# Kernel optimization log

Hardware: AMD Instinct MI355X
Metric: run time of the kernel (lower is better)

The kernel has to match this reference:

```python
import jax, jax.numpy as jnp
import numpy as np

N_NODES = 100000
N_EDGES = 1600000
IN_F, HID, N_COLORS = 128, 128, 10


def setup_inputs() -> dict:
    key = jax.random.key(0)
    k1, k2, k3, k4 = jax.random.split(key, 4)
    x = jax.random.normal(k1, (N_NODES, IN_F), dtype=jnp.float32)
    edge_index = jax.random.randint(k2, (2, N_EDGES), 0, N_NODES, dtype=jnp.int64)
    # Glorot-ish init for weights
    W1 = jax.random.normal(k3, (IN_F, HID), dtype=jnp.float32) / np.sqrt(IN_F)
    b1 = jnp.zeros((HID,), dtype=jnp.float32)
    W2 = jax.random.normal(k4, (HID, N_COLORS), dtype=jnp.float32) / np.sqrt(HID)
    b2 = jnp.zeros((N_COLORS,), dtype=jnp.float32)
    return {"x": x, "edge_index": edge_index, "W1": W1, "b1": b1, "W2": W2, "b2": b2}


def _gcn_norm(edge_index, num_nodes):
    # Add self-loops, compute symmetric normalization D^-1/2 (A+I) D^-1/2
    loops = jnp.arange(num_nodes, dtype=edge_index.dtype)
    src = jnp.concatenate([edge_index[0], loops])
    dst = jnp.concatenate([edge_index[1], loops])
    deg = jax.ops.segment_sum(jnp.ones_like(dst, dtype=jnp.float32), dst,
                              num_segments=num_nodes)
    deg_isqrt = jax.lax.rsqrt(deg)  # deg >= 1 due to self-loops
    norm = deg_isqrt[src] * deg_isqrt[dst]  # [E + N]
    return src, dst, norm


def _gcn_conv(h, src, dst, norm, num_nodes, W, b):
    # Linear transform first (PyG GCNConv), then gather-scale-scatter aggregate
    h = h @ W                                   # [N, out]
    msg = h[src] * norm[:, None]                # [E + N, out] gather
    out = jax.ops.segment_sum(msg, dst, num_segments=num_nodes)  # scatter-add
    return out + b


def reference(x, edge_index, W1, b1, W2, b2):
    n = x.shape[0]
    src, dst, norm = _gcn_norm(edge_index, n)
    h = _gcn_conv(x, src, dst, norm, n, W1, b1)
    h = jax.nn.relu(h)
    # dropout is identity in eval mode
    h = _gcn_conv(h, src, dst, norm, n, W2, b2)
    return jax.nn.softmax(h, axis=1)
```

## Files before the change

### kernel.cpp

```cpp
#include <hip/hip_runtime.h>
#include <hip/hip_fp16.h>

#define IN_F 128
#define HID  128
#define NC   10
#define H2P  16
#define NPB  128
#define NBMAX 784
#define BCAP 2560
#define CAPP 2944
#define EPB  4096
#define LDW  136

typedef _Float16 f16x8 __attribute__((ext_vector_type(8)));
typedef float f32x4 __attribute__((ext_vector_type(4)));
typedef int int4a __attribute__((ext_vector_type(4), aligned(4)));

__device__ inline __half2 shfl_xor_h2(__half2 v, int mask) {
    int i = __shfl_xor(*reinterpret_cast<int*>(&v), mask, 64);
    return *reinterpret_cast<__half2*>(&i);
}

__global__ __launch_bounds__(1024) void k_bin(const int* __restrict__ src,
                                              const int* __restrict__ dst,
                                              int* __restrict__ bcnt,
                                              unsigned int* __restrict__ binned,
                                              const float* __restrict__ W1,
                                              __half* __restrict__ WT,
                                              const float* __restrict__ W2,
                                              float* __restrict__ W2T,
                                              int E, int nbin) {
    __shared__ int hist[NBMAX];
    __shared__ int base[NBMAX];
    __shared__ int lcur[NBMAX];
    const int tid = threadIdx.x;

    if (blockIdx.x == 0) {
        for (int i = tid; i < IN_F * HID; i += 1024) {
            int k = i >> 7, n = i & 127;
            WT[n * IN_F + k] = __float2half(W1[k * HID + n]);
        }
        for (int i = tid; i < NC * IN_F; i += 1024)
            W2T[i] = W2[(i & 127) * NC + (i >> 7)];
    }

    for (int b = tid; b < nbin; b += 1024) { hist[b] = 0; lcur[b] = 0; }
    __syncthreads();

    const int e0 = blockIdx.x * EPB + tid;
    int d[4];
    #pragma unroll
    for (int u = 0; u < 4; u++) {
        int e = e0 + u * 1024;
        d[u] = (e < E) ? dst[e] : -1;
        if (d[u] >= 0) atomicAdd(&hist[d[u] >> 7], 1);
    }
    __syncthreads();
    for (int b = tid; b < nbin; b += 1024) {
        int h = hist[b];
        base[b] = h ? atomicAdd(&bcnt[b], h) : 0;
    }
    __syncthreads();
    #pragma unroll
    for (int u = 0; u < 4; u++) {
        int e = e0 + u * 1024;
        if (e < E) {
            int dd = d[u];
            int b = dd >> 7;
            int s = src[e];
            int o = base[b] + atomicAdd(&lcur[b], 1);
            if (o < BCAP)
                binned[(size_t)b * BCAP + o] = ((unsigned)(dd & 127) << 17) | (unsigned)s;
        }
    }
}

__global__ __launch_bounds__(256) void k_pg(const int* __restrict__ bcnt,
                                            const unsigned int* __restrict__ binned,
                                            int2* __restrict__ rowinfo,
                                            float* __restrict__ dis,
                                            int* __restrict__ csr,
                                            const float* __restrict__ X,
                                            const __half* __restrict__ WT,
                                            __half* __restrict__ hsh,
                                            __half* __restrict__ h2h,
                                            int N) {
    __shared__ int h[NPB];
    __shared__ int lb[NPB];
    __shared__ int cur[NPB];
    __shared__ float sdis[NPB];
    __shared__ _Float16 sX[32 * LDW];
    __shared__ _Float16 sW[128 * LDW];
    const int b = blockIdx.x;
    const int tid = threadIdx.x;

    if (tid < NPB) h[tid] = 0;
    __syncthreads();

    const int m = min(bcnt[b], BCAP);
    const unsigned int* p = binned + (size_t)b * BCAP;
    for (int i = tid; i < m; i += 256) atomicAdd(&h[p[i] >> 17], 1);
    __syncthreads();

    int myh = 0, cnt4 = 0;
    if (tid < NPB) { myh = h[tid]; cnt4 = (myh + 3) & ~3; lb[tid] = cnt4; }
    __syncthreads();
    #pragma unroll
    for (int off = 1; off < NPB; off <<= 1) {
        int t = (tid < NPB && tid >= off) ? lb[tid - off] : 0;
        __syncthreads();
        if (tid < NPB) lb[tid] += t;
        __syncthreads();
    }
    int ex = 0;
    if (tid < NPB) {
        ex = lb[tid] - cnt4;
        int node = b * NPB + tid;
        if (node < N) {
            rowinfo[node] = make_int2(b * CAPP + ex, cnt4);
            float dd = rsqrtf(1.0f + (float)myh);
            dis[node] = dd;
            sdis[tid] = dd;
        }
        lb[tid] = ex;
        cur[tid] = 0;
    }
    __syncthreads();
    for (int i = tid; i < m; i += 256) {
        unsigned v = p[i];
        int dl = v >> 17;
        int r = atomicAdd(&cur[dl], 1);
        csr[b * CAPP + lb[dl] + r] = (int)(v & 0x1FFFF);
    }
    if (tid < NPB) {
        for (int k = myh; k < cnt4; k++) csr[b * CAPP + ex + k] = N;
    }
    if (b == 0) {
        f16x8 z = {0, 0, 0, 0, 0, 0, 0, 0};
        if (tid < 16) *(f16x8*)(hsh + (size_t)N * HID + tid * 8) = z;
        if (tid < 2)  *(f16x8*)(h2h + (size_t)N * H2P + tid * 8) = z;
    }

    {
        int n = tid >> 1, part = tid & 1;
        const f16x8* srcp = (const f16x8*)(WT + n * IN_F + part * 64);
        f16x8* dstp = (f16x8*)(sW + n * LDW + part * 64);
        #pragma unroll
        for (int c = 0; c < 8; c++) dstp[c] = srcp[c];
    }
    const int wave = tid >> 6;
    const int lane = tid & 63;
    const int quad = lane >> 4;
    const int l16 = lane & 15;
    const int nbase = wave * 32;

    for (int tdx = 0; tdx < 4; tdx++) {
        int row0 = b * NPB + tdx * 32;
        if (row0 >= N) break;
        __syncthreads();
        {
            int r = tid >> 3;
            int k0 = (tid & 7) * 16;
            const float* sp = X + (size_t)(row0 + r) * IN_F + k0;
            float4 f0 = *(const float4*)(sp);
            float4 f1 = *(const float4*)(sp + 4);
            float4 f2 = *(const float4*)(sp + 8);
            float4 f3 = *(const float4*)(sp + 12);
            f16x8 h0, h1;
            h0[0] = (_Float16)f0.x; h0[1] = (_Float16)f0.y;
            h0[2] = (_Float16)f0.z; h0[3] = (_Float16)f0.w;
            h0[4] = (_Float16)f1.x; h0[5] = (_Float16)f1.y;
            h0[6] = (_Float16)f1.z; h0[7] = (_Float16)f1.w;
            h1[0] = (_Float16)f2.x; h1[1] = (_Float16)f2.y;
            h1[2] = (_Float16)f2.z; h1[3] = (_Float16)f2.w;
            h1[4] = (_Float16)f3.x; h1[5] = (_Float16)f3.y;
            h1[6] = (_Float16)f3.z; h1[7] = (_Float16)f3.w;
            *(f16x8*)(sX + r * LDW + k0) = h0;
            *(f16x8*)(sX + r * LDW + k0 + 8) = h1;
        }
        __syncthreads();

        f32x4 acc00 = {0,0,0,0}, acc01 = {0,0,0,0}, acc10 = {0,0,0,0}, acc11 = {0,0,0,0};
        #pragma unroll
        for (int kc = 0; kc < 4; kc++) {
            const int koff = kc * 32 + quad * 8;
            f16x8 a0 = *(const f16x8*)(sX + l16 * LDW + koff);
            f16x8 a1 = *(const f16x8*)(sX + (16 + l16) * LDW + koff);
            f16x8 b0 = *(const f16x8*)(sW + (nbase + l16) * LDW + koff);
            f16x8 b1 = *(const f16x8*)(sW + (nbase + 16 + l16) * LDW + koff);
            acc00 = __builtin_amdgcn_mfma_f32_16x16x32_f16(a0, b0, acc00, 0, 0, 0);
            acc01 = __builtin_amdgcn_mfma_f32_16x16x32_f16(a0, b1, acc01, 0, 0, 0);
            acc10 = __builtin_amdgcn_mfma_f32_16x16x32_f16(a1, b0, acc10, 0, 0, 0);
            acc11 = __builtin_amdgcn_mfma_f32_16x16x32_f16(a1, b1, acc11, 0, 0, 0);
        }
        #pragma unroll
        for (int r = 0; r < 4; r++) {
            {
                int lr = tdx * 32 + quad * 4 + r;
                float d = sdis[lr];
                __half* o = hsh + (size_t)(b * NPB + lr) * HID + nbase + l16;
                o[0]  = __float2half(acc00[r] * d);
                o[16] = __float2half(acc01[r] * d);
            }
            {
                int lr = tdx * 32 + 16 + quad * 4 + r;
                float d = sdis[lr];
                __half* o = hsh + (size_t)(b * NPB + lr) * HID + nbase + l16;
                o[0]  = __float2half(acc10[r] * d);
                o[16] = __float2half(acc11[r] * d);
            }
        }
    }
}

__global__ __launch_bounds__(256) void k_agg1(const __half* __restrict__ hsh,
                                              const int2* __restrict__ rowinfo,
                                              const int* __restrict__ csr,
                                              const float* __restrict__ dis,
                                              const float* __restrict__ b1,
                                              const float* __restrict__ W2T,
                                              __half* __restrict__ h2h,
                                              int N) {
    const int node = blockIdx.x * 4 + (threadIdx.x >> 6);
    if (node >= N) return;
    const int lane = threadIdx.x & 63;
    const int g   = lane >> 4;
    const int l16 = lane & 15;
    const int f0  = l16 * 8;
    const __half2 hz = __half2half2(__float2half(0.0f));

    const int2 ri = rowinfo[node];
    const int beg = ri.x, end = ri.x + ri.y;
    const float d = dis[node];

    __half2 acc2[4] = {hz, hz, hz, hz};
    if (g == 0) {
        float4 r = *(const float4*)(hsh + (size_t)node * HID + f0);
        const __half2* hh = (const __half2*)&r;
        acc2[0] = hh[0]; acc2[1] = hh[1]; acc2[2] = hh[2]; acc2[3] = hh[3];
    }

    int j0 = beg + 4 * g;
    if (j0 < end) {
        int4a cv0 = *(const int4a*)(csr + j0);
        int  j1 = j0 + 16;
        bool m1 = j1 < end;
        int4a cv1 = m1 ? *(const int4a*)(csr + j1) : cv0;
        float4 r0 = *(const float4*)(hsh + (size_t)cv0[0] * HID + f0);
        float4 r1 = *(const float4*)(hsh + (size_t)cv0[1] * HID + f0);
        float4 r2 = *(const float4*)(hsh + (size_t)cv0[2] * HID + f0);
        float4 r3 = *(const float4*)(hsh + (size_t)cv0[3] * HID + f0);
        while (true) {
            const int  j2 = j1 + 16;
            const bool m2 = m1 && (j2 < end);
            int4a cv2 = m2 ? *(const int4a*)(csr + j2) : cv1;
            float4 n0, n1, n2, n3;
            if (m1) {
                n0 = *(const float4*)(hsh + (size_t)cv1[0] * HID + f0);
                n1 = *(const float4*)(hsh + (size_t)cv1[1] * HID + f0);
                n2 = *(const float4*)(hsh + (size_t)cv1[2] * HID + f0);
                n3 = *(const float4*)(hsh + (size_t)cv1[3] * HID + f0);
            }
            const __half2* h0 = (const __half2*)&r0;
            const __half2* h1 = (const __half2*)&r1;
            const __half2* h2 = (const __half2*)&r2;
            const __half2* h3 = (const __half2*)&r3;
            #pragma unroll
            for (int i = 0; i < 4; i++) {
                acc2[i] = __hadd2(acc2[i], h0[i]);
                acc2[i] = __hadd2(acc2[i], h1[i]);
                acc2[i] = __hadd2(acc2[i], h2[i]);
                acc2[i] = __hadd2(acc2[i], h3[i]);
            }
            if (!m1) break;
            r0 = n0; r1 = n1; r2 = n2; r3 = n3;
            cv1 = cv2; m1 = m2; j1 = j2;
        }
    }

    #pragma unroll
    for (int i = 0; i < 4; i++) {
        acc2[i] = __hadd2(acc2[i], shfl_xor_h2(acc2[i], 16));
        acc2[i] = __hadd2(acc2[i], shfl_xor_h2(acc2[i], 32));
    }
    float acc[8];
    #pragma unroll
    for (int i = 0; i < 4; i++) {
        float2 t = __half22float2(acc2[i]);
        acc[2 * i] = t.x; acc[2 * i + 1] = t.y;
    }

    float4 ba = *(const float4*)(b1 + f0);
    float4 bb = *(const float4*)(b1 + f0 + 4);
    float h[8];
    h[0] = fmaxf(fmaf(d, acc[0], ba.x), 0.0f);
    h[1] = fmaxf(fmaf(d, acc[1], ba.y), 0.0f);
    h[2] = fmaxf(fmaf(d, acc[2], ba.z), 0.0f);
    h[3] = fmaxf(fmaf(d, acc[3], ba.w), 0.0f);
    h[4] = fmaxf(fmaf(d, acc[4], bb.x), 0.0f);
    h[5] = fmaxf(fmaf(d, acc[5], bb.y), 0.0f);
    h[6] = fmaxf(fmaf(d, acc[6], bb.z), 0.0f);
    h[7] = fmaxf(fmaf(d, acc[7], bb.w), 0.0f);

    const int cb = (g == 0) ? 0 : (g == 1) ? 3 : (g == 2) ? 6 : 8;
    const int nc = (g < 2) ? 3 : 2;
    float p[3];
    #pragma unroll
    for (int ci = 0; ci < 3; ci++) {
        if (ci < nc) {
            int c = cb + ci;
            float4 wa = *(const float4*)(W2T + c * IN_F + f0);
            float4 wb = *(const float4*)(W2T + c * IN_F + f0 + 4);
            float t = fmaf(h[0], wa.x, fmaf(h[1], wa.y, fmaf(h[2], wa.z, h[3] * wa.w)));
            t = fmaf(h[4], wb.x, fmaf(h[5], wb.y, fmaf(h[6], wb.z, fmaf(h[7], wb.w, t))));
            #pragma unroll
            for (int off = 1; off < 16; off <<= 1) t += __shfl_xor(t, off, 64);
            p[ci] = t;
        }
    }
    if (l16 == 0) {
        __half* o = h2h + (size_t)node * H2P + cb;
        for (int ci = 0; ci < nc; ci++) o[ci] = __float2half(d * p[ci]);
    }
}

__global__ __launch_bounds__(256) void k_agg2(const __half* __restrict__ h2h,
                                              const int2* __restrict__ rowinfo,
                                              const int* __restrict__ csr,
                                              const float* __restrict__ dis,
                                              const float* __restrict__ b2,
                                              float* __restrict__ out,
                                              int N) {
    int t = blockIdx.x * 256 + threadIdx.x;
    int node = t >> 3;
    if (node >= N) return;
    int o = t & 7;
    int q = o & 1;
    int eg = o >> 1;
    const int base = q * 8;
    const __half2 hz = __half2half2(__float2half(0.0f));

    __half2 a2[4] = {hz, hz, hz, hz};
    if (eg == 0) {
        float4 r = *(const float4*)(h2h + (size_t)node * H2P + base);
        const __half2* hh = (const __half2*)&r;
        a2[0] = hh[0]; a2[1] = hh[1]; a2[2] = hh[2]; a2[3] = hh[3];
    }
    const int2 ri = rowinfo[node];
    const int end = ri.x + ri.y;

    int j0 = ri.x + 4 * eg;
    if (j0 < end) {
        int4a cv0 = *(const int4a*)(csr + j0);
        int  j1 = j0 + 16;
        bool m1 = j1 < end;
        int4a cv1 = m1 ? *(const int4a*)(csr + j1) : cv0;
        float4 r0 = *(const float4*)(h2h + (size_t)cv0[0] * H2P + base);
        float4 r1 = *(const float4*)(h2h + (size_t)cv0[1] * H2P + base);
        float4 r2 = *(const float4*)(h2h + (size_t)cv0[2] * H2P + base);
        float4 r3 = *(const float4*)(h2h + (size_t)cv0[3] * H2P + base);
        while (true) {
            const int  j2 = j1 + 16;
            const bool m2 = m1 && (j2 < end);
            int4a cv2 = m2 ? *(const int4a*)(csr + j2) : cv1;
            float4 n0, n1, n2, n3;
            if (m1) {
                n0 = *(const float4*)(h2h + (size_t)cv1[0] * H2P + base);
                n1 = *(const float4*)(h2h + (size_t)cv1[1] * H2P + base);
                n2 = *(const float4*)(h2h + (size_t)cv1[2] * H2P + base);
                n3 = *(const float4*)(h2h + (size_t)cv1[3] * H2P + base);
            }
            const __half2* h0 = (const __half2*)&r0;
            const __half2* h1 = (const __half2*)&r1;
            const __half2* h2 = (const __half2*)&r2;
            const __half2* h3 = (const __half2*)&r3;
            #pragma unroll
            for (int i = 0; i < 4; i++) {
                a2[i] = __hadd2(a2[i], h0[i]);
                a2[i] = __hadd2(a2[i], h1[i]);
                a2[i] = __hadd2(a2[i], h2[i]);
                a2[i] = __hadd2(a2[i], h3[i]);
            }
            if (!m1) break;
            r0 = n0; r1 = n1; r2 = n2; r3 = n3;
            cv1 = cv2; m1 = m2; j1 = j2;
        }
    }

    #pragma unroll
    for (int i = 0; i < 4; i++) {
        a2[i] = __hadd2(a2[i], shfl_xor_h2(a2[i], 2));
        a2[i] = __hadd2(a2[i], shfl_xor_h2(a2[i], 4));
    }

    float a[8];
    #pragma unroll
    for (int i = 0; i < 4; i++) {
        float2 tt = __half22float2(a2[i]);
        a[2 * i] = tt.x; a[2 * i + 1] = tt.y;
    }

    const float d = dis[node];
    float vv[8];
    #pragma unroll
    for (int i = 0; i < 8; i++) {
        int f = base + i;
        vv[i] = (f < NC) ? fmaf(d, a[i], b2[f]) : -1e30f;
    }
    float m = vv[0];
    #pragma unroll
    for (int i = 1; i < 8; i++) m = fmaxf(m, vv[i]);
    m = fmaxf(m, __shfl_xor(m, 1, 64));
    float e[8];
    float s = 0.0f;
    #pragma unroll
    for (int i = 0; i < 8; i++) { e[i] = (base + i < NC) ? expf(vv[i] - m) : 0.0f; s += e[i]; }
    s += __shfl_xor(s, 1, 64);
    float inv = 1.0f / s;

    float* op = out + (size_t)node * NC;
    if (o == 0) {
        *(float2*)(op + 0) = make_float2(e[0] * inv, e[1] * inv);
        *(float2*)(op + 2) = make_float2(e[2] * inv, e[3] * inv);
        *(float2*)(op + 4) = make_float2(e[4] * inv, e[5] * inv);
        *(float2*)(op + 6) = make_float2(e[6] * inv, e[7] * inv);
    } else if (o == 1) {
        *(float2*)(op + 8) = make_float2(e[0] * inv, e[1] * inv);
    }
}

extern "C" void kernel_launch(void* const* d_in, const int* in_sizes, int n_in,
                              void* d_out, int out_size, void* d_ws, size_t ws_size,
                              hipStream_t stream) {
    const float* x  = (const float*)d_in[0];
    const int*   ei = (const int*)d_in[1];
    const float* W1 = (const float*)d_in[2];
    const float* b1 = (const float*)d_in[3];
    const float* W2 = (const float*)d_in[4];
    const float* b2 = (const float*)d_in[5];
    float* out = (float*)d_out;

    const int N = in_sizes[0] / IN_F;
    const int E = in_sizes[1] / 2;
    const int* esrc = ei;
    const int* edst = ei + E;
    const int nbin = (N + NPB - 1) / NPB;

    char* ws = (char*)d_ws;
    int2*   rowinfo = (int2*)(ws);
    float*  dis     = (float*)(ws + 0x100000);
    int*    bcnt    = (int*)(ws + 0x180000);
    __half* WT      = (__half*)(ws + 0x190000);
    float*  W2T     = (float*)(ws + 0x1A0000);
    unsigned int* binned = (unsigned int*)(ws + 0x200000);
    int*    csr     = (int*)(ws + 0xA00000);
    __half* hsh     = (__half*)(ws + 0x1400000);
    __half* h2h     = (__half*)(ws + 0x2D00000);

    hipMemsetAsync(bcnt, 0, (size_t)nbin * sizeof(int), stream);

    k_bin <<<(E + EPB - 1) / EPB, 1024, 0, stream>>>(esrc, edst, bcnt, binned, W1, WT, W2, W2T, E, nbin);
    k_pg  <<<nbin, 256, 0, stream>>>(bcnt, binned, rowinfo, dis, csr, x, WT, hsh, h2h, N);
    k_agg1<<<(N + 3) / 4, 256, 0, stream>>>(hsh, rowinfo, csr, dis, b1, W2T, h2h, N);
    k_agg2<<<(int)(((size_t)N * 8 + 255) / 256), 256, 0, stream>>>(h2h, rowinfo, csr, dis, b2, out, N);
}
```

Measured before the change: 231.1 us.

## Double k_pg block size to 512 threads and split k_agg1 into two launches

k_pg now runs 512 threads per block. Two 256-thread halves each stage a 32-row X tile into separate shared buffers, so the dense transform covers two row tiles per pass with 8 waves. Row indices are clamped on load and guarded on store. k_agg1 is parameterized by a node range and launched twice over the two halves of the nodes, which adds launch overhead and gains no obvious parallelism since both launches share one stream. Shared memory per block grows by one X tile, which may lower occupancy.

```diff
diff --git a/kernel.cpp b/kernel.cpp
--- a/kernel.cpp
+++ b/kernel.cpp
@@ -75,7 +75,7 @@
     }
 }
 
-__global__ __launch_bounds__(256) void k_pg(const int* __restrict__ bcnt,
+__global__ __launch_bounds__(512) void k_pg(const int* __restrict__ bcnt,
                                             const unsigned int* __restrict__ binned,
                                             int2* __restrict__ rowinfo,
                                             float* __restrict__ dis,
@@ -89,7 +89,7 @@
     __shared__ int lb[NPB];
     __shared__ int cur[NPB];
     __shared__ float sdis[NPB];
-    __shared__ _Float16 sX[32 * LDW];
+    __shared__ _Float16 sX[2][32 * LDW];
     __shared__ _Float16 sW[128 * LDW];
     const int b = blockIdx.x;
     const int tid = threadIdx.x;
@@ -99,7 +99,7 @@
 
     const int m = min(bcnt[b], BCAP);
     const unsigned int* p = binned + (size_t)b * BCAP;
-    for (int i = tid; i < m; i += 256) atomicAdd(&h[p[i] >> 17], 1);
+    for (int i = tid; i < m; i += 512) atomicAdd(&h[p[i] >> 17], 1);
     __syncthreads();
 
     int myh = 0, cnt4 = 0;
@@ -126,7 +126,7 @@
         cur[tid] = 0;
     }
     __syncthreads();
-    for (int i = tid; i < m; i += 256) {
+    for (int i = tid; i < m; i += 512) {
         unsigned v = p[i];
         int dl = v >> 17;
         int r = atomicAdd(&cur[dl], 1);
@@ -142,26 +142,31 @@
     }
 
     {
-        int n = tid >> 1, part = tid & 1;
-        const f16x8* srcp = (const f16x8*)(WT + n * IN_F + part * 64);
-        f16x8* dstp = (f16x8*)(sW + n * LDW + part * 64);
+        int n = tid >> 2, part = tid & 3;
+        const f16x8* srcp = (const f16x8*)(WT + n * IN_F);
+        f16x8* dstp = (f16x8*)(sW + n * LDW);
         #pragma unroll
-        for (int c = 0; c < 8; c++) dstp[c] = srcp[c];
-    }
+        for (int c = 0; c < 4; c++) dstp[part * 4 + c] = srcp[part * 4 + c];
+    }
+
     const int wave = tid >> 6;
+    const int grp  = wave >> 2;
+    const int nbase = (wave & 3) * 32;
     const int lane = tid & 63;
     const int quad = lane >> 4;
     const int l16 = lane & 15;
-    const int nbase = wave * 32;
-
-    for (int tdx = 0; tdx < 4; tdx++) {
-        int row0 = b * NPB + tdx * 32;
-        if (row0 >= N) break;
+    const int sub256 = tid >> 8;
+    const int t256 = tid & 255;
+
+    for (int t = 0; t < 2; t++) {
         __syncthreads();
         {
-            int r = tid >> 3;
-            int k0 = (tid & 7) * 16;
-            const float* sp = X + (size_t)(row0 + r) * IN_F + k0;
+            int tdx = 2 * t + sub256;
+            int r = t256 >> 3;
+            int k0 = (t256 & 7) * 16;
+            int row = b * NPB + tdx * 32 + r;
+            if (row >= N) row = N - 1;
+            const float* sp = X + (size_t)row * IN_F + k0;
             float4 f0 = *(const float4*)(sp);
             float4 f1 = *(const float4*)(sp + 4);
             float4 f2 = *(const float4*)(sp + 8);
@@ -175,17 +180,18 @@
             h1[2] = (_Float16)f2.z; h1[3] = (_Float16)f2.w;
             h1[4] = (_Float16)f3.x; h1[5] = (_Float16)f3.y;
             h1[6] = (_Float16)f3.z; h1[7] = (_Float16)f3.w;
-            *(f16x8*)(sX + r * LDW + k0) = h0;
-            *(f16x8*)(sX + r * LDW + k0 + 8) = h1;
+            *(f16x8*)(sX[sub256] + r * LDW + k0) = h0;
+            *(f16x8*)(sX[sub256] + r * LDW + k0 + 8) = h1;
         }
         __syncthreads();
 
+        const int tdx = 2 * t + grp;
         f32x4 acc00 = {0,0,0,0}, acc01 = {0,0,0,0}, acc10 = {0,0,0,0}, acc11 = {0,0,0,0};
         #pragma unroll
         for (int kc = 0; kc < 4; kc++) {
             const int koff = kc * 32 + quad * 8;
-            f16x8 a0 = *(const f16x8*)(sX + l16 * LDW + koff);
-            f16x8 a1 = *(const f16x8*)(sX + (16 + l16) * LDW + koff);
+            f16x8 a0 = *(const f16x8*)(sX[grp] + l16 * LDW + koff);
+            f16x8 a1 = *(const f16x8*)(sX[grp] + (16 + l16) * LDW + koff);
             f16x8 b0 = *(const f16x8*)(sW + (nbase + l16) * LDW + koff);
             f16x8 b1 = *(const f16x8*)(sW + (nbase + 16 + l16) * LDW + koff);
             acc00 = __builtin_amdgcn_mfma_f32_16x16x32_f16(a0, b0, acc00, 0, 0, 0);
@@ -197,17 +203,23 @@
         for (int r = 0; r < 4; r++) {
             {
                 int lr = tdx * 32 + quad * 4 + r;
-                float d = sdis[lr];
-                __half* o = hsh + (size_t)(b * NPB + lr) * HID + nbase + l16;
-                o[0]  = __float2half(acc00[r] * d);
-                o[16] = __float2half(acc01[r] * d);
+                int row = b * NPB + lr;
+                if (row < N) {
+                    float d = sdis[lr];
+                    __half* o = hsh + (size_t)row * HID + nbase + l16;
+                    o[0]  = __float2half(acc00[r] * d);
+                    o[16] = __float2half(acc01[r] * d);
+                }
             }
             {
                 int lr = tdx * 32 + 16 + quad * 4 + r;
-                float d = sdis[lr];
-                __half* o = hsh + (size_t)(b * NPB + lr) * HID + nbase + l16;
-                o[0]  = __float2half(acc10[r] * d);
-                o[16] = __float2half(acc11[r] * d);
+                int row = b * NPB + lr;
+                if (row < N) {
+                    float d = sdis[lr];
+                    __half* o = hsh + (size_t)row * HID + nbase + l16;
+                    o[0]  = __float2half(acc10[r] * d);
+                    o[16] = __float2half(acc11[r] * d);
+                }
             }
         }
     }
@@ -220,9 +232,9 @@
                                               const float* __restrict__ b1,
                                               const float* __restrict__ W2T,
                                               __half* __restrict__ h2h,
-                                              int N) {
-    const int node = blockIdx.x * 4 + (threadIdx.x >> 6);
-    if (node >= N) return;
+                                              int base0, int nend) {
+    const int node = base0 + blockIdx.x * 4 + (threadIdx.x >> 6);
+    if (node >= nend) return;
     const int lane = threadIdx.x & 63;
     const int g   = lane >> 4;
     const int l16 = lane & 15;
@@ -460,7 +472,9 @@
     hipMemsetAsync(bcnt, 0, (size_t)nbin * sizeof(int), stream);
 
     k_bin <<<(E + EPB - 1) / EPB, 1024, 0, stream>>>(esrc, edst, bcnt, binned, W1, WT, W2, W2T, E, nbin);
-    k_pg  <<<nbin, 256, 0, stream>>>(bcnt, binned, rowinfo, dis, csr, x, WT, hsh, h2h, N);
-    k_agg1<<<(N + 3) / 4, 256, 0, stream>>>(hsh, rowinfo, csr, dis, b1, W2T, h2h, N);
+    k_pg  <<<nbin, 512, 0, stream>>>(bcnt, binned, rowinfo, dis, csr, x, WT, hsh, h2h, N);
+    const int half = ((N / 2) + 3) & ~3;
+    k_agg1<<<(half + 3) / 4, 256, 0, stream>>>(hsh, rowinfo, csr, dis, b1, W2T, h2h, 0, half);
+    k_agg1<<<((N - half) + 3) / 4, 256, 0, stream>>>(hsh, rowinfo, csr, dis, b1, W2T, h2h, half, N);
     k_agg2<<<(int)(((size_t)N * 8 + 255) / 256), 256, 0, stream>>>(h2h, rowinfo, csr, dis, b2, out, N);
 }
```

Result: no change. 232.2 us (+0.5%).
